# Kernel tuning notes

Measured on AMD Instinct MI355X. Metric: run time of the kernel, lower is better.

The kernel has to match this reference:

```python
import jax, jax.numpy as jnp
import numpy as np
from jax import lax

BBOX_XFORM_CLIP = float(np.log(1000.0 / 16.0))
PRE_NMS_TOP_K = 1000
SCORE_THRESH = 0.05
IOU_THRESH = 0.5
MAX_DET = 100


def _decode_boxes(encoded, anchors):
    # encoded [...,4] = [dy,dx,dh,dw] with weights [10,10,5,5]; anchors [...,4] = [y1,x1,y2,x2]
    dy = encoded[..., 0] / 10.0
    dx = encoded[..., 1] / 10.0
    dh = jnp.minimum(encoded[..., 2] / 5.0, BBOX_XFORM_CLIP)
    dw = jnp.minimum(encoded[..., 3] / 5.0, BBOX_XFORM_CLIP)
    ah = anchors[..., 2] - anchors[..., 0]
    aw = anchors[..., 3] - anchors[..., 1]
    ayc = anchors[..., 0] + 0.5 * ah
    axc = anchors[..., 1] + 0.5 * aw
    yc = dy * ah + ayc
    xc = dx * aw + axc
    h = jnp.exp(dh) * ah
    w = jnp.exp(dw) * aw
    return jnp.stack([yc - 0.5 * h, xc - 0.5 * w, yc + 0.5 * h, xc + 0.5 * w], axis=-1)


def _clip_boxes(boxes, image_shape):
    # boxes [B,N,4]; image_shape [B,2] = (height, width)
    h = image_shape[..., 0:1]
    w = image_shape[..., 1:2]
    maxlen = jnp.concatenate([h, w, h, w], axis=-1)[:, None, :]  # [B,1,4]
    return jnp.clip(boxes, 0.0, maxlen)


def _nms_keep(boxes):
    # Greedy sequential NMS on score-sorted boxes [k,4]; returns keep mask [k].
    k = boxes.shape[0]
    y1, x1, y2, x2 = boxes[:, 0], boxes[:, 1], boxes[:, 2], boxes[:, 3]
    area = (y2 - y1) * (x2 - x1)
    idxs = jnp.arange(k)

    def body(keep, i):
        iy1 = jnp.maximum(y1[i], y1)
        ix1 = jnp.maximum(x1[i], x1)
        iy2 = jnp.minimum(y2[i], y2)
        ix2 = jnp.minimum(x2[i], x2)
        inter = jnp.maximum(iy2 - iy1, 0.0) * jnp.maximum(ix2 - ix1, 0.0)
        union = area[i] + area - inter
        iou = inter / jnp.where(union > 0, union, 1.0)
        suppressed = jnp.any(keep & (idxs < i) & (iou > IOU_THRESH))
        return keep.at[i].set(~suppressed), None

    keep, _ = lax.scan(body, jnp.zeros((k,), jnp.bool_), idxs)
    return keep


def _nms_single(boxes, scores):
    # boxes [k,4], scores [k] sorted descending; mirrors sorted_non_max_suppression_padded output.
    keep = _nms_keep(lax.stop_gradient(boxes))
    valid = keep & jnp.any(boxes > 0, axis=-1)  # zeroed (filtered) boxes never count
    sel = jnp.where(valid, scores, -jnp.inf)
    top_s, top_i = lax.top_k(sel, MAX_DET)
    out_valid = top_s > -jnp.inf
    out_scores = jnp.where(out_valid, top_s, 0.0)
    out_boxes = boxes[top_i] * out_valid[:, None].astype(boxes.dtype)
    return out_scores, out_boxes


def setup_inputs() -> dict:
    key = jax.random.key(0)
    k1, k2, k3, k4 = jax.random.split(key, 4)
    B, K, C = 8, 8192, 91
    raw_boxes = jax.random.normal(k1, (B, K, C * 4), jnp.float32) * 0.5
    raw_scores = jax.random.normal(k2, (B, K, C), jnp.float32) * 2.0
    # valid anchors [y1,x1,y2,x2] inside a 1024x1024 image
    ctr = jax.random.uniform(k3, (B, K, 2), jnp.float32, 0.0, 1024.0)
    sz = jax.random.uniform(k4, (B, K, 2), jnp.float32, 16.0, 128.0)
    anchor_boxes = jnp.concatenate([ctr - 0.5 * sz, ctr + 0.5 * sz], axis=-1)
    image_shape = jnp.full((B, 2), 1024.0, jnp.float32)
    return {"raw_boxes": raw_boxes, "raw_scores": raw_scores,
            "anchor_boxes": anchor_boxes, "image_shape": image_shape}


def reference(raw_boxes, raw_scores, anchor_boxes, image_shape):
    B, K, C = raw_scores.shape
    Cc = C - 1  # background removed

    probs = jax.nn.softmax(raw_scores, axis=-1)[:, :, 1:]           # [B,K,Cc]
    boxes = raw_boxes.reshape(B, K, C, 4)[:, :, 1:, :]              # [B,K,Cc,4]
    anch = jnp.broadcast_to(anchor_boxes[:, :, None, :], boxes.shape)
    dec = _decode_boxes(boxes.reshape(B, K * Cc, 4), anch.reshape(B, K * Cc, 4))
    dec = _clip_boxes(dec, image_shape).reshape(B, K, Cc, 4)

    # per-class top-k pre-NMS candidates (_select_top_k_scores + gather)
    k = min(K, PRE_NMS_TOP_K)
    s_t = jnp.transpose(probs, (0, 2, 1))                           # [B,Cc,K]
    top_s, top_i = lax.top_k(s_t, k)                                # [B,Cc,k]
    b_t = jnp.transpose(dec, (0, 2, 1, 3))                          # [B,Cc,K,4]
    top_b = jnp.take_along_axis(b_t, top_i[..., None], axis=2)      # [B,Cc,k,4]

    # filter_boxes_by_scores: score -> -1, box -> 0 below threshold
    mask = top_s > SCORE_THRESH
    top_s = jnp.where(mask, top_s, -1.0)
    top_b = top_b * mask[..., None].astype(top_b.dtype)

    nms_s, nms_b = jax.vmap(jax.vmap(_nms_single))(top_b, top_s)    # [B,Cc,MAX_DET], [B,Cc,MAX_DET,4]
    classes = jnp.broadcast_to(jnp.arange(Cc, dtype=jnp.int32)[None, :, None], nms_s.shape)

    all_s = nms_s.reshape(B, Cc * MAX_DET)
    all_b = nms_b.reshape(B, Cc * MAX_DET, 4)
    all_c = classes.reshape(B, Cc * MAX_DET)

    fin_s, fin_i = lax.top_k(all_s, MAX_DET)
    fin_b = jnp.take_along_axis(all_b, fin_i[..., None], axis=1)
    fin_c = jnp.take_along_axis(all_c, fin_i, axis=1) + 1           # restore background offset
    num = jnp.sum((fin_s > -1.0).astype(jnp.int32), axis=1)
    return fin_b, fin_s, fin_c, num
```

## Files before the change

### kernel.cpp

```cpp
#include <hip/hip_runtime.h>
#include <stdint.h>

typedef unsigned long long ull;

#define K_ANCH   8192
#define NCLS     91
#define NCC      90
#define B_SZ     8
#define CAP      1024
#define PRE_NMS  1000
#define MAXDET   100
#define CHUNK    64
#define NWMAX    16
#define NBW      128
#define SCORE_TH 0.05f
#define IOU_TH   0.5f
#define BBOX_CLIP 4.1351665565490723f

__device__ __forceinline__ float wave_max64(float v) {
  #pragma unroll
  for (int off = 32; off > 0; off >>= 1) v = fmaxf(v, __shfl_xor(v, off, 64));
  return v;
}
__device__ __forceinline__ float wave_sum64(float v) {
  #pragma unroll
  for (int off = 32; off > 0; off >>= 1) v += __shfl_xor(v, off, 64);
  return v;
}

__device__ __forceinline__ float4 decode_clip(float4 e, float4 a, float imh, float imw) {
#pragma clang fp contract(off)
  float dy = e.x / 10.0f;
  float dx = e.y / 10.0f;
  float dh = fminf(e.z / 5.0f, BBOX_CLIP);
  float dw = fminf(e.w / 5.0f, BBOX_CLIP);
  float ah = a.z - a.x;
  float aw = a.w - a.y;
  float ayc = a.x + 0.5f * ah;
  float axc = a.y + 0.5f * aw;
  float yc = dy * ah + ayc;
  float xc = dx * aw + axc;
  float h = expf(dh) * ah;
  float w = expf(dw) * aw;
  float y1 = yc - 0.5f * h, x1 = xc - 0.5f * w;
  float y2 = yc + 0.5f * h, x2 = xc + 0.5f * w;
  y1 = fminf(fmaxf(y1, 0.0f), imh);
  x1 = fminf(fmaxf(x1, 0.0f), imw);
  y2 = fminf(fmaxf(y2, 0.0f), imh);
  x2 = fminf(fmaxf(x2, 0.0f), imw);
  return make_float4(y1, x1, y2, x2);
}

__device__ __forceinline__ bool iou_gt(float4 bi, float ai, float4 bj, float aj) {
#pragma clang fp contract(off)
  float iy1 = fmaxf(bi.x, bj.x);
  float ix1 = fmaxf(bi.y, bj.y);
  float iy2 = fminf(bi.z, bj.z);
  float ix2 = fminf(bi.w, bj.w);
  float inter = fmaxf(iy2 - iy1, 0.0f) * fmaxf(ix2 - ix1, 0.0f);
  float uni = ai + aj - inter;
  float iou = inter / (uni > 0.0f ? uni : 1.0f);
  return iou > IOU_TH;
}

__global__ __launch_bounds__(1024) void kT_softmax(
    const float* __restrict__ raw_scores,
    float2* __restrict__ stats, ull* __restrict__ bmask)
{
  __shared__ ull rowbits[64][2];
  int tid = threadIdx.x;
  int wv = tid >> 6, lane = tid & 63;
  int b = blockIdx.x >> 7;
  int k0 = (blockIdx.x & 127) << 6;
  #pragma unroll
  for (int i = 0; i < 4; i++) {
    int rl = (wv << 2) + i;
    int row = b * K_ANCH + k0 + rl;
    const float* srow = raw_scores + (size_t)row * NCLS;
    float s0 = srow[lane];
    bool has1 = lane < (NCLS - 64);
    float s1 = has1 ? srow[64 + lane] : -INFINITY;
    float m = wave_max64(fmaxf(s0, s1));
    float e0 = expf(s0 - m);
    float e1 = has1 ? expf(s1 - m) : 0.0f;
    float denom = wave_sum64(e0 + e1);
    ull b0 = __ballot(lane >= 1 && (e0 / denom) > SCORE_TH);
    ull b1 = __ballot(has1 && (e1 / denom) > SCORE_TH);
    if (lane == 0) {
      stats[row] = make_float2(m, denom);
      rowbits[rl][0] = b0;
      rowbits[rl][1] = b1;
    }
  }
  __syncthreads();
  if (tid < NCC) {
    int c = tid + 1, w = c >> 6, bit = c & 63;
    ull out = 0;
    #pragma unroll
    for (int r = 0; r < 64; r++)
      out |= ((rowbits[r][w] >> bit) & 1ull) << r;
    bmask[(size_t)(b * NCC + tid) * NBW + (k0 >> 6)] = out;
  }
}

__global__ __launch_bounds__(256) void kN_nms(
    const float* __restrict__ raw_boxes, const float* __restrict__ raw_scores,
    const float* __restrict__ anchors, const float* __restrict__ image_shape,
    const float2* __restrict__ stats, const ull* __restrict__ bmask,
    float* __restrict__ all_s, float4* __restrict__ all_b)
{
  __shared__ float4 sbox[PRE_NMS];
  __shared__ float  sarea[PRE_NMS];
  __shared__ float  sscore[PRE_NMS];
  __shared__ ull    sbuf[1056];
  __shared__ int    soff[NBW];
  __shared__ int    swtot[2];
  __shared__ int    s_n;
  __shared__ int    s_done;
#define SMASK(w, r) sbuf[(w) * (CHUNK + 1) + (r)]

  int bc  = blockIdx.x;
  int tid = threadIdx.x;
  int b = bc / NCC;
  int c = bc - b * NCC + 1;
  int outbase = bc * MAXDET;

  for (int i = tid; i < MAXDET; i += 256) {
    all_s[outbase + i] = 0.0f;
    all_b[outbase + i] = make_float4(0.f, 0.f, 0.f, 0.f);
  }

  ull w0 = 0;
  int cnt = 0;
  if (tid < NBW) { w0 = bmask[(size_t)bc * NBW + tid]; cnt = __popcll(w0); }
  int incl = cnt;
  if (tid < 128) {
    int lane = tid & 63;
    #pragma unroll
    for (int d = 1; d < 64; d <<= 1) {
      int o = __shfl_up(incl, d, 64);
      if (lane >= d) incl += o;
    }
    if (lane == 63) swtot[tid >> 6] = incl;
  }
  if (tid == 0) s_done = 0;
  __syncthreads();
  if (tid < 128) soff[tid] = incl - cnt + ((tid >= 64) ? swtot[0] : 0);
  if (tid == 0) s_n = swtot[0] + swtot[1];
  __syncthreads();
  int n_load = min(s_n, CAP);

  if (tid < NBW) {
    int slot = soff[tid];
    ull m = w0;
    int kb = tid << 6;
    while (m) {
      int bit = __ffsll(m) - 1;
      m &= m - 1;
      if (slot < CAP) sbuf[slot] = (ull)(kb + bit);
      slot++;
    }
  }
  __syncthreads();

  size_t rowb = (size_t)b * K_ANCH;
  for (int i = tid; i < n_load; i += 256) {
    int k = (int)sbuf[i];
    size_t row = rowb + k;
    float s = raw_scores[row * NCLS + c];
    float2 md = stats[row];
    float p = expf(s - md.x) / md.y;
    sbuf[i] = ((ull)__float_as_uint(p) << 32) | (uint32_t)(K_ANCH - 1 - k);
  }
  int n2 = (n_load <= 512) ? 512 : 1024;
  for (int i = n_load + tid; i < n2; i += 256) sbuf[i] = 0ull;
  __syncthreads();

  if (n_load <= 512) {
    ull e0 = sbuf[tid], e1 = sbuf[tid + 256];
    for (int size = 2; size <= 512; size <<= 1) {
      if (size == 512 && e0 < e1) { ull t = e0; e0 = e1; e1 = t; }
      for (int s = ((size >> 1) > 128 ? 128 : (size >> 1)); s >= 64; s >>= 1) {
        __syncthreads();
        sbuf[tid] = e0; sbuf[tid + 256] = e1;
        __syncthreads();
        ull p0 = sbuf[tid ^ s];
        ull p1 = sbuf[(tid + 256) ^ s];
        bool t0 = (((tid & s) == 0) == ((tid & size) == 0));
        bool t1 = ((((tid + 256) & s) == 0) == (((tid + 256) & size) == 0));
        e0 = t0 ? (e0 > p0 ? e0 : p0) : (e0 < p0 ? e0 : p0);
        e1 = t1 ? (e1 > p1 ? e1 : p1) : (e1 < p1 ? e1 : p1);
      }
      int smax = ((size >> 1) < 32 ? (size >> 1) : 32);
      for (int s = smax; s >= 1; s >>= 1) {
        ull p0 = __shfl_xor(e0, s, 64);
        ull p1 = __shfl_xor(e1, s, 64);
        bool t0 = (((tid & s) == 0) == ((tid & size) == 0));
        bool t1 = ((((tid + 256) & s) == 0) == (((tid + 256) & size) == 0));
        e0 = t0 ? (e0 > p0 ? e0 : p0) : (e0 < p0 ? e0 : p0);
        e1 = t1 ? (e1 > p1 ? e1 : p1) : (e1 < p1 ? e1 : p1);
      }
    }
    __syncthreads();
    sbuf[tid] = e0;
    sbuf[tid + 256] = e1;
    __syncthreads();
  } else {
    for (int size = 2; size <= 1024; size <<= 1) {
      for (int stride = size >> 1; stride > 0; stride >>= 1) {
        for (int i = tid; i < 1024; i += 256) {
          int j = i ^ stride;
          if (j > i) {
            ull ki = sbuf[i], kj = sbuf[j];
            bool desc = ((i & size) == 0);
            if (desc ? (ki < kj) : (ki > kj)) { sbuf[i] = kj; sbuf[j] = ki; }
          }
        }
        __syncthreads();
      }
    }
  }

  int n_use = min(n_load, PRE_NMS);
  float imh = image_shape[b * 2 + 0];
  float imw = image_shape[b * 2 + 1];
  for (int i = tid; i < n_use; i += 256) {
    ull key = sbuf[i];
    int k = K_ANCH - 1 - (int)(key & 0xFFFFFFFFull);
    size_t row = rowb + k;
    float4 e = ((const float4*)raw_boxes)[row * NCLS + c];
    float4 a = ((const float4*)anchors)[row];
    float4 box = decode_clip(e, a, imh, imw);
    sbox[i] = box;
    sscore[i] = __uint_as_float((uint32_t)(key >> 32));
    {
#pragma clang fp contract(off)
      sarea[i] = (box.z - box.x) * (box.w - box.y);
    }
  }

  int nwords = (n_use + 63) >> 6;
  ull rem = 0;
  int written = 0;
  for (int c0 = 0; c0 < n_use; c0 += CHUNK) {
    __syncthreads();
    if (s_done) break;
    int nrows = min(CHUNK, n_use - c0);

    for (int p = tid; p < (nwords << 6); p += 256) {
      int w  = p >> 6;
      int rr = p & (CHUNK - 1);
      if (rr >= nrows) continue;
      int r = c0 + rr;
      float4 br = sbox[r];
      float  ar = sarea[r];
      int j0 = w << 6;
      int j1 = min(j0 + 64, n_use);
      int js = max(j0, r + 1);
      ull mrow = 0;
      for (int j = js; j < j1; j++) {
        if (iou_gt(br, ar, sbox[j], sarea[j])) mrow |= 1ull << (j - j0);
      }
      SMASK(w, rr) = mrow;
    }
    __syncthreads();

    if (tid < 64) {
      int lane = tid;
      for (int i = c0; i < c0 + nrows; i++) {
        int w = i >> 6, bit = i & 63;
        ull rw = __shfl(rem, w, 64);
        if (((rw >> bit) & 1ull) == 0) {
          if (lane < nwords) rem |= SMASK(lane, i - c0);
          int valid = 0;
          float4 bx;
          float sc = 0.f;
          if (lane == 0) {
            bx = sbox[i];
            valid = (bx.x > 0.f || bx.y > 0.f || bx.z > 0.f || bx.w > 0.f) ? 1 : 0;
            sc = sscore[i];
          }
          valid = __shfl(valid, 0, 64);
          if (valid) {
            if (lane == 0) {
              all_s[outbase + written] = sc;
              all_b[outbase + written] = bx;
            }
            written++;
            if (written == MAXDET) {
              if (lane == 0) s_done = 1;
              break;
            }
          }
        }
      }
    }
  }
#undef SMASK
}

__global__ __launch_bounds__(256) void k3_final(
    const float* __restrict__ all_s, const float4* __restrict__ all_b,
    float* __restrict__ out)
{
  __shared__ float ss[NCC * MAXDET];
  int b = blockIdx.x;
  int tid = threadIdx.x;
  const float* S = all_s + (size_t)b * NCC * MAXDET;
  for (int i = tid; i < NCC * MAXDET; i += 256) ss[i] = S[i];
  __syncthreads();
  if (tid >= 64) return;
  int lane = tid;

  float* fin_b = out;
  float* fin_s = out + B_SZ * MAXDET * 4;
  float* fin_c = fin_s + B_SZ * MAXDET;
  float* numo  = fin_c + B_SZ * MAXDET;

  int c0 = lane;
  int c1 = lane + 64;
  int p0 = 0, p1 = 0;
  ull cur0 = ((ull)__float_as_uint(ss[c0 * MAXDET]) << 32) | (uint32_t)(16383 - c0 * MAXDET);
  ull nxt0 = ((ull)__float_as_uint(ss[c0 * MAXDET + 1]) << 32) | (uint32_t)(16383 - (c0 * MAXDET + 1));
  ull cur1 = 0ull, nxt1 = 0ull;
  if (c1 < NCC) {
    cur1 = ((ull)__float_as_uint(ss[c1 * MAXDET]) << 32) | (uint32_t)(16383 - c1 * MAXDET);
    nxt1 = ((ull)__float_as_uint(ss[c1 * MAXDET + 1]) << 32) | (uint32_t)(16383 - (c1 * MAXDET + 1));
  }
  int cnt = 0;

  for (int step = 0; step < MAXDET; step++) {
    ull my = (cur0 > cur1) ? cur0 : cur1;
    ull g = my;
    #pragma unroll
    for (int off = 32; off > 0; off >>= 1) {
      ull o = __shfl_xor(g, off, 64);
      g = (o > g) ? o : g;
    }
    if (cur0 != 0ull && g == cur0) {
      p0++;
      cur0 = nxt0;
      int f = c0 * MAXDET + p0 + 1;
      nxt0 = (p0 + 1 < MAXDET)
           ? (((ull)__float_as_uint(ss[f]) << 32) | (uint32_t)(16383 - f)) : 0ull;
    } else if (cur1 != 0ull && g == cur1) {
      p1++;
      cur1 = nxt1;
      int f = c1 * MAXDET + p1 + 1;
      nxt1 = (p1 + 1 < MAXDET)
           ? (((ull)__float_as_uint(ss[f]) << 32) | (uint32_t)(16383 - f)) : 0ull;
    }

    if (lane == 0) {
      int flat = 16383 - (int)(g & 0xFFFFFFFFull);
      int cc = flat / MAXDET;
      float sc = __uint_as_float((uint32_t)(g >> 32));
      fin_s[b * MAXDET + step] = sc;
      fin_c[b * MAXDET + step] = (float)(cc + 1);
      float4 bx = all_b[(size_t)b * NCC * MAXDET + flat];
      ((float4*)fin_b)[b * MAXDET + step] = bx;
      if (sc > -1.0f) cnt++;
    }
  }
  if (lane == 0) numo[b] = (float)cnt;
}

extern "C" void kernel_launch(void* const* d_in, const int* in_sizes, int n_in,
                              void* d_out, int out_size, void* d_ws, size_t ws_size,
                              hipStream_t stream) {
  const float* raw_boxes   = (const float*)d_in[0];
  const float* raw_scores  = (const float*)d_in[1];
  const float* anchors     = (const float*)d_in[2];
  const float* image_shape = (const float*)d_in[3];

  char* p = (char*)d_ws;
  auto alloc = [&](size_t bytes) {
    char* r = p;
    p += (bytes + 255) & ~(size_t)255;
    return r;
  };
  float2* stats = (float2*)alloc((size_t)B_SZ * K_ANCH * sizeof(float2));
  ull*    bmask = (ull*)   alloc((size_t)B_SZ * NCC * NBW * sizeof(ull));
  float*  all_s = (float*) alloc((size_t)B_SZ * NCC * MAXDET * sizeof(float));
  float4* all_b = (float4*)alloc((size_t)B_SZ * NCC * MAXDET * sizeof(float4));

  kT_softmax<<<B_SZ * 128, 1024, 0, stream>>>(raw_scores, stats, bmask);
  kN_nms<<<B_SZ * NCC, 256, 0, stream>>>(raw_boxes, raw_scores, anchors, image_shape,
                                         stats, bmask, all_s, all_b);
  k3_final<<<B_SZ, 256, 0, stream>>>(all_s, all_b, (float*)d_out);
}
```

Measured before the change: 303.2 us.

## Stage above-threshold probabilities and decoded boxes in softmax kernel for NMS

The softmax kernel now builds a per-block worklist of (class, anchor) pairs whose probability passes the score threshold. For each it writes the probability and the decoded, clipped box into compact per-class, per-64-anchor staging buffers sized by a capacity chosen from workspace size. The NMS kernel then reads these contiguous staged values instead of re-gathering strided raw_scores, stats and raw_boxes, falling back to the original path when the rank exceeds the capacity. This trades extra shared memory (about 24KB for a probability tile plus the worklist) and more global writes in the first kernel for fewer scattered reads in the per-class NMS kernel.

```diff
diff --git a/kernel.cpp b/kernel.cpp
--- a/kernel.cpp
+++ b/kernel.cpp
@@ -64,14 +64,22 @@
 }
 
 __global__ __launch_bounds__(1024) void kT_softmax(
-    const float* __restrict__ raw_scores,
-    float2* __restrict__ stats, ull* __restrict__ bmask)
+    const float* __restrict__ raw_scores, const float* __restrict__ raw_boxes,
+    const float4* __restrict__ anchors, const float* __restrict__ image_shape,
+    float2* __restrict__ stats, ull* __restrict__ bmask,
+    float* __restrict__ pstage, float4* __restrict__ bstage, int pcap)
 {
-  __shared__ ull rowbits[64][2];
+  __shared__ ull    rowbits[64][2];
+  __shared__ float  sp[64][92];
+  __shared__ float4 sanch[64];
+  __shared__ int    wl[5760];
+  __shared__ int    wl_n;
   int tid = threadIdx.x;
   int wv = tid >> 6, lane = tid & 63;
   int b = blockIdx.x >> 7;
   int k0 = (blockIdx.x & 127) << 6;
+  if (tid == 0) wl_n = 0;
+  if (tid < 64) sanch[tid] = anchors[(size_t)b * K_ANCH + k0 + tid];
   #pragma unroll
   for (int i = 0; i < 4; i++) {
     int rl = (wv << 2) + i;
@@ -84,8 +92,12 @@
     float e0 = expf(s0 - m);
     float e1 = has1 ? expf(s1 - m) : 0.0f;
     float denom = wave_sum64(e0 + e1);
-    ull b0 = __ballot(lane >= 1 && (e0 / denom) > SCORE_TH);
-    ull b1 = __ballot(has1 && (e1 / denom) > SCORE_TH);
+    float p0 = e0 / denom;
+    float p1 = e1 / denom;
+    sp[rl][lane] = p0;
+    if (has1) sp[rl][64 + lane] = p1;
+    ull b0 = __ballot(lane >= 1 && p0 > SCORE_TH);
+    ull b1 = __ballot(has1 && p1 > SCORE_TH);
     if (lane == 0) {
       stats[row] = make_float2(m, denom);
       rowbits[rl][0] = b0;
@@ -100,19 +112,50 @@
     for (int r = 0; r < 64; r++)
       out |= ((rowbits[r][w] >> bit) & 1ull) << r;
     bmask[(size_t)(b * NCC + tid) * NBW + (k0 >> 6)] = out;
+    int cnt = __popcll(out);
+    if (cnt > 0) {
+      int basei = atomicAdd(&wl_n, cnt);
+      ull m = out;
+      int rank = 0;
+      while (m) {
+        int r = __ffsll(m) - 1;
+        m &= m - 1;
+        wl[basei + rank] = (c << 12) | (r << 6) | rank;
+        rank++;
+      }
+    }
+  }
+  __syncthreads();
+  int nwl = wl_n;
+  if (pcap > 0) {
+    float imh = image_shape[b * 2 + 0];
+    float imw = image_shape[b * 2 + 1];
+    for (int t = tid; t < nwl; t += 1024) {
+      int e = wl[t];
+      int c = e >> 12, r = (e >> 6) & 63, rank = e & 63;
+      if (rank >= pcap) continue;
+      size_t row = (size_t)b * K_ANCH + k0 + r;
+      float4 enc = ((const float4*)raw_boxes)[row * NCLS + c];
+      float4 box = decode_clip(enc, sanch[r], imh, imw);
+      size_t pw = (size_t)(b * NCC + (c - 1)) * NBW + (k0 >> 6);
+      pstage[pw * pcap + rank] = sp[r][c];
+      bstage[pw * pcap + rank] = box;
+    }
   }
 }
 
 __global__ __launch_bounds__(256) void kN_nms(
     const float* __restrict__ raw_boxes, const float* __restrict__ raw_scores,
-    const float* __restrict__ anchors, const float* __restrict__ image_shape,
+    const float4* __restrict__ anchors, const float* __restrict__ image_shape,
     const float2* __restrict__ stats, const ull* __restrict__ bmask,
+    const float* __restrict__ pstage, const float4* __restrict__ bstage, int pcap,
     float* __restrict__ all_s, float4* __restrict__ all_b)
 {
   __shared__ float4 sbox[PRE_NMS];
   __shared__ float  sarea[PRE_NMS];
   __shared__ float  sscore[PRE_NMS];
   __shared__ ull    sbuf[1056];
+  __shared__ ull    sbm[NBW];
   __shared__ int    soff[NBW];
   __shared__ int    swtot[2];
   __shared__ int    s_n;
@@ -124,6 +167,7 @@
   int b = bc / NCC;
   int c = bc - b * NCC + 1;
   int outbase = bc * MAXDET;
+  size_t rowb = (size_t)b * K_ANCH;
 
   for (int i = tid; i < MAXDET; i += 256) {
     all_s[outbase + i] = 0.0f;
@@ -132,7 +176,11 @@
 
   ull w0 = 0;
   int cnt = 0;
-  if (tid < NBW) { w0 = bmask[(size_t)bc * NBW + tid]; cnt = __popcll(w0); }
+  if (tid < NBW) {
+    w0 = bmask[(size_t)bc * NBW + tid];
+    sbm[tid] = w0;
+    cnt = __popcll(w0);
+  }
   int incl = cnt;
   if (tid < 128) {
     int lane = tid & 63;
@@ -154,23 +202,26 @@
     int slot = soff[tid];
     ull m = w0;
     int kb = tid << 6;
+    int rank = 0;
+    size_t pw = (size_t)bc * NBW + tid;
     while (m) {
       int bit = __ffsll(m) - 1;
       m &= m - 1;
-      if (slot < CAP) sbuf[slot] = (ull)(kb + bit);
+      int k = kb + bit;
+      float p;
+      if (rank < pcap) {
+        p = pstage[pw * (size_t)pcap + rank];
+      } else {
+        size_t row = rowb + k;
+        float s = raw_scores[row * NCLS + c];
+        float2 md = stats[row];
+        p = expf(s - md.x) / md.y;
+      }
+      if (slot < CAP)
+        sbuf[slot] = ((ull)__float_as_uint(p) << 32) | (uint32_t)(K_ANCH - 1 - k);
       slot++;
-    }
-  }
-  __syncthreads();
-
-  size_t rowb = (size_t)b * K_ANCH;
-  for (int i = tid; i < n_load; i += 256) {
-    int k = (int)sbuf[i];
-    size_t row = rowb + k;
-    float s = raw_scores[row * NCLS + c];
-    float2 md = stats[row];
-    float p = expf(s - md.x) / md.y;
-    sbuf[i] = ((ull)__float_as_uint(p) << 32) | (uint32_t)(K_ANCH - 1 - k);
+      rank++;
+    }
   }
   int n2 = (n_load <= 512) ? 512 : 1024;
   for (int i = n_load + tid; i < n2; i += 256) sbuf[i] = 0ull;
@@ -227,10 +278,16 @@
   for (int i = tid; i < n_use; i += 256) {
     ull key = sbuf[i];
     int k = K_ANCH - 1 - (int)(key & 0xFFFFFFFFull);
-    size_t row = rowb + k;
-    float4 e = ((const float4*)raw_boxes)[row * NCLS + c];
-    float4 a = ((const float4*)anchors)[row];
-    float4 box = decode_clip(e, a, imh, imw);
+    int w = k >> 6;
+    int rank = __popcll(sbm[w] & ((1ull << (k & 63)) - 1ull));
+    float4 box;
+    if (rank < pcap) {
+      box = bstage[((size_t)bc * NBW + w) * (size_t)pcap + rank];
+    } else {
+      size_t row = rowb + k;
+      float4 e = ((const float4*)raw_boxes)[row * NCLS + c];
+      box = decode_clip(e, anchors[row], imh, imw);
+    }
     sbox[i] = box;
     sscore[i] = __uint_as_float((uint32_t)(key >> 32));
     {
@@ -368,15 +425,16 @@
 extern "C" void kernel_launch(void* const* d_in, const int* in_sizes, int n_in,
                               void* d_out, int out_size, void* d_ws, size_t ws_size,
                               hipStream_t stream) {
-  const float* raw_boxes   = (const float*)d_in[0];
-  const float* raw_scores  = (const float*)d_in[1];
-  const float* anchors     = (const float*)d_in[2];
-  const float* image_shape = (const float*)d_in[3];
+  const float*  raw_boxes   = (const float*)d_in[0];
+  const float*  raw_scores  = (const float*)d_in[1];
+  const float4* anchors     = (const float4*)d_in[2];
+  const float*  image_shape = (const float*)d_in[3];
 
   char* p = (char*)d_ws;
+  size_t used = 0;
   auto alloc = [&](size_t bytes) {
-    char* r = p;
-    p += (bytes + 255) & ~(size_t)255;
+    char* r = p + used;
+    used += (bytes + 255) & ~(size_t)255;
     return r;
   };
   float2* stats = (float2*)alloc((size_t)B_SZ * K_ANCH * sizeof(float2));
@@ -384,8 +442,17 @@
   float*  all_s = (float*) alloc((size_t)B_SZ * NCC * MAXDET * sizeof(float));
   float4* all_b = (float4*)alloc((size_t)B_SZ * NCC * MAXDET * sizeof(float4));
 
-  kT_softmax<<<B_SZ * 128, 1024, 0, stream>>>(raw_scores, stats, bmask);
+  size_t nw = (size_t)B_SZ * NCC * NBW;
+  int pcap = 16;
+  while (pcap > 0 && used + ((nw * pcap * 4 + 255) & ~(size_t)255)
+                          + ((nw * pcap * 16 + 255) & ~(size_t)255) > ws_size)
+    pcap >>= 1;
+  float*  pstage = (float*) alloc(nw * (size_t)pcap * 4);
+  float4* bstage = (float4*)alloc(nw * (size_t)pcap * 16);
+
+  kT_softmax<<<B_SZ * 128, 1024, 0, stream>>>(raw_scores, raw_boxes, anchors, image_shape,
+                                              stats, bmask, pstage, bstage, pcap);
   kN_nms<<<B_SZ * NCC, 256, 0, stream>>>(raw_boxes, raw_scores, anchors, image_shape,
-                                         stats, bmask, all_s, all_b);
+                                         stats, bmask, pstage, bstage, pcap, all_s, all_b);
   k3_final<<<B_SZ, 256, 0, stream>>>(all_s, all_b, (float*)d_out);
 }
```

Result: slower. 311.8 us (+2.8%).
